# Optimization experiments

Measured on AMD Instinct MI355X. Metric: run time of the kernel, lower is better.

Reference implementation:

```python
import math
import jax, jax.numpy as jnp
import numpy as np

B, C, T, H, FC, L, K, S, O = 4, 512, 2048, 8, 2048, 6, 3, 256, 1
DK = C // H


def _conv1x1(x, w, b):
    # x: (B,Cin,T), w: (Cout,Cin)
    return jnp.einsum('oc,bct->bot', w, x) + b[None, :, None]


def _conv1d(x, w, b, pad):
    # x: (B,Cin,T), w: (Cout,Cin,K), pad: (left,right)
    y = jax.lax.conv_general_dilated(x, w, (1,), [pad],
                                     dimension_numbers=('NCH', 'OIH', 'NCH'))
    return y + b[None, :, None]


def _layernorm_c(x, g, b, eps=1e-5):
    # LayerNorm over channel dim (module transposes to put channels last)
    m = jnp.mean(x, axis=1, keepdims=True)
    v = jnp.mean((x - m) ** 2, axis=1, keepdims=True)
    return (x - m) * jax.lax.rsqrt(v + eps) * g[None, :, None] + b[None, :, None]


def _attention(x, qw, qb, kw, kb, vw, vb, ow, ob, tri):
    b_, c, t = x.shape
    # reshape(b, H, dk, t).transpose(2,3) -> (B,H,T,dk)
    q = _conv1x1(x, qw, qb).reshape(b_, H, DK, t).transpose(0, 1, 3, 2)
    k = _conv1x1(x, kw, kb).reshape(b_, H, DK, t).transpose(0, 1, 3, 2)
    v = _conv1x1(x, vw, vb).reshape(b_, H, DK, t).transpose(0, 1, 3, 2)
    scores = jnp.einsum('bhtd,bhsd->bhts', q, k) / math.sqrt(DK)
    scores = jnp.where(tri, scores, -1e4)  # causal mask, matches Tensor.where(mask, s, -10000)
    p = jax.nn.softmax(scores, axis=-1)
    o = jnp.einsum('bhts,bhsd->bhtd', p, v)
    o = o.transpose(0, 1, 3, 2).reshape(b_, c, t)
    return _conv1x1(o, ow, ob)


def _ffn(x, x_mask, w1, b1, w2, b2):
    # causal FFN: left pad K-1, activation=None -> relu, p_dropout=0
    y = _conv1d(x * x_mask, w1, b1, (K - 1, 0))
    y = jax.nn.relu(y)
    return _conv1d(y * x_mask, w2, b2, (K - 1, 0)) * x_mask


def _forward(x, norm_f0, x_mask, spk_emb,
             prenet_w, prenet_b, f0pre_w, f0pre_b, cond_w, cond_b, proj_w, proj_b,
             qw, qb, kw, kb, vw, vb, ow, ob,
             ln0_g, ln0_b, ln1_g, ln1_b,
             ffn1_w, ffn1_b, ffn2_w, ffn2_b):
    x = jax.lax.stop_gradient(x)  # torch.detach(x)
    x = x + _conv1x1(spk_emb, cond_w, cond_b)
    x = x + _conv1d(norm_f0, f0pre_w, f0pre_b, (1, 1))
    x = _conv1d(x, prenet_w, prenet_b, (1, 1)) * x_mask
    t = x.shape[2]
    tri = jnp.tril(jnp.ones((t, t), dtype=bool))[None, None]  # subsequent_mask
    x = x * x_mask
    for i in range(L):
        y = _attention(x, qw[i], qb[i], kw[i], kb[i], vw[i], vb[i], ow[i], ob[i], tri)
        x = _layernorm_c(x + y, ln0_g[i], ln0_b[i])
        y = _ffn(x, x_mask, ffn1_w[i], ffn1_b[i], ffn2_w[i], ffn2_b[i])
        x = _layernorm_c(x + y, ln1_g[i], ln1_b[i])
    x = x * x_mask
    return _conv1x1(x, proj_w, proj_b) * x_mask


def setup_inputs() -> dict:
    key = jax.random.key(0)
    ks = iter(jax.random.split(key, 40))
    rn = lambda shape, scale: jax.random.normal(next(ks), shape, jnp.float32) * scale
    inp = {
        'x': rn((B, C, T), 1.0),
        'norm_f0': rn((B, 1, T), 1.0),
        'x_mask': jnp.ones((B, 1, T), jnp.float32),
        'spk_emb': rn((B, S, T), 1.0),
        'prenet_w': rn((C, C, K), (C * K) ** -0.5), 'prenet_b': jnp.zeros((C,), jnp.float32),
        'f0pre_w': rn((C, 1, K), K ** -0.5), 'f0pre_b': jnp.zeros((C,), jnp.float32),
        'cond_w': rn((C, S), S ** -0.5), 'cond_b': jnp.zeros((C,), jnp.float32),
        'proj_w': rn((O, C), C ** -0.5), 'proj_b': jnp.zeros((O,), jnp.float32),
        'qw': rn((L, C, C), C ** -0.5), 'qb': jnp.zeros((L, C), jnp.float32),
        'kw': rn((L, C, C), C ** -0.5), 'kb': jnp.zeros((L, C), jnp.float32),
        'vw': rn((L, C, C), C ** -0.5), 'vb': jnp.zeros((L, C), jnp.float32),
        'ow': rn((L, C, C), C ** -0.5), 'ob': jnp.zeros((L, C), jnp.float32),
        'ln0_g': jnp.ones((L, C), jnp.float32), 'ln0_b': jnp.zeros((L, C), jnp.float32),
        'ln1_g': jnp.ones((L, C), jnp.float32), 'ln1_b': jnp.zeros((L, C), jnp.float32),
        'ffn1_w': rn((L, FC, C, K), (C * K) ** -0.5), 'ffn1_b': jnp.zeros((L, FC), jnp.float32),
        'ffn2_w': rn((L, C, FC, K), (FC * K) ** -0.5), 'ffn2_b': jnp.zeros((L, C), jnp.float32),
    }
    return inp


def reference(x, norm_f0, x_mask, spk_emb,
              prenet_w, prenet_b, f0pre_w, f0pre_b, cond_w, cond_b, proj_w, proj_b,
              qw, qb, kw, kb, vw, vb, ow, ob,
              ln0_g, ln0_b, ln1_g, ln1_b,
              ffn1_w, ffn1_b, ffn2_w, ffn2_b):
    return _forward(x, norm_f0, x_mask, spk_emb,
                    prenet_w, prenet_b, f0pre_w, f0pre_b, cond_w, cond_b, proj_w, proj_b,
                    qw, qb, kw, kb, vw, vb, ow, ob,
                    ln0_g, ln0_b, ln1_g, ln1_b,
                    ffn1_w, ffn1_b, ffn2_w, ffn2_b)
```

## Files before the change

kernel.cpp:

```cpp
#include <hip/hip_runtime.h>
#include <cstdint>
#include <cstddef>

#define T_LEN 2048
#define B_SZ 4
#define C_CH 512
#define H_N 8
#define DK_ 64
#define FC_CH 2048
#define L_N 6
#define KW 3
#define S_CH 256

typedef _Float16 h8 __attribute__((ext_vector_type(8)));
typedef _Float16 h4 __attribute__((ext_vector_type(4)));
typedef float floatx4 __attribute__((ext_vector_type(4)));

__global__ __launch_bounds__(256)
void cast_f16(const float* __restrict__ src, _Float16* __restrict__ dst, int n)
{
    int i = blockIdx.x * 256 + threadIdx.x;
    if (i < n) dst[i] = (_Float16)src[i];
}

__global__ __launch_bounds__(256)
void prepack_k3(const float* __restrict__ src, _Float16* __restrict__ dst,
                int Cin, int total)
{
    int i = blockIdx.x * 256 + threadIdx.x;
    if (i >= total) return;
    const int rk = Cin * 3;
    int row = i / rk, o = i - row * rk;
    int blk = o / 96, rr = o - blk * 96;
    int k = rr >> 5, cl = rr & 31;
    dst[i] = (_Float16)src[(size_t)row * rk + (size_t)(blk * 32 + cl) * 3 + k];
}

__global__ __launch_bounds__(256)
void prepack_qkv(const float* __restrict__ qw, const float* __restrict__ kw,
                 const float* __restrict__ vw, const float* __restrict__ qb,
                 const float* __restrict__ kb, const float* __restrict__ vb,
                 _Float16* __restrict__ dst, float* __restrict__ bdst)
{
    int i = blockIdx.x * 256 + threadIdx.x;
    const int total = L_N * 1536 * 512;
    if (i < total) {
        int l = i / (1536 * 512);
        int o = i - l * (1536 * 512);
        int m = o >> 9, c = o & 511;
        const float* s = (m < 512) ? qw : ((m < 1024) ? kw : vw);
        dst[i] = (_Float16)s[((size_t)l * 512 + (m & 511)) * 512 + c];
    }
    if (i < L_N * 1536) {
        int l = i / 1536, m = i - l * 1536;
        const float* s = (m < 512) ? qb : ((m < 1024) ? kb : vb);
        bdst[i] = s[l * 512 + (m & 511)];
    }
}

__global__ __launch_bounds__(256)
void transpose_f0(const float* __restrict__ src, _Float16* __restrict__ dst, int Cd,
                  const float* __restrict__ nf0, const float* __restrict__ f0w,
                  const float* __restrict__ f0b, int do_f0)
{
    __shared__ float tile[32][33];
    const int tl = threadIdx.x & 31;
    const int r  = threadIdx.x >> 5;
    const int t00 = blockIdx.x * 32;
    const int c00 = blockIdx.y * 32;
    const int b   = blockIdx.z;
    const float* s0 = src + (size_t)b * Cd * T_LEN;
#pragma unroll
    for (int rr = 0; rr < 4; ++rr) {
        int cl = r + rr * 8;
        tile[cl][tl] = s0[(size_t)(c00 + cl) * T_LEN + t00 + tl];
    }
    __syncthreads();
    _Float16* d0 = dst + (size_t)b * T_LEN * Cd;
    const int cg = c00 + tl;
#pragma unroll
    for (int rr = 0; rr < 4; ++rr) {
        int tlo = r + rr * 8;
        float v = tile[tl][tlo];
        if (do_f0) {
            int tg = t00 + tlo;
            float a = f0b[cg];
#pragma unroll
            for (int k = 0; k < 3; ++k) {
                int gt = tg + k - 1;
                if (gt >= 0 && gt < T_LEN) a += f0w[cg * 3 + k] * nf0[(size_t)b * T_LEN + gt];
            }
            v += a;
        }
        d0[(size_t)(t00 + tlo) * Cd + cg] = (_Float16)v;
    }
}

template<int KK, int OUTMODE>
__global__ __launch_bounds__(256)
void conv_gemm_mfma(const _Float16* __restrict__ in, const _Float16* __restrict__ Wpk,
                    const float* __restrict__ bias, const _Float16* __restrict__ res,
                    const float* __restrict__ mask, _Float16* __restrict__ out_v,
                    _Float16* __restrict__ out2,
                    int Cin, int out_stride, int pl, int do_relu,
                    int mask_in, int mask_out)
{
    constexpr int CS   = (KK == 3) ? 32 : 64;
    constexpr int NSEC = (KK == 3) ? 3 : 2;
    constexpr int AST  = NSEC * 32 + 8;
    constexpr int HALO = (KK == 3) ? 2 : 0;
    constexpr int RB   = 128 + 2 * HALO;
    constexpr int BST  = CS + 8;
    constexpr int NAH  = NSEC * 2;
    constexpr int NTASK = RB * (CS / 16);
    __shared__ _Float16 sA[128 * AST];
    __shared__ _Float16 sB[RB * BST];

    const int tid = threadIdx.x;
    const int lane = tid & 63;
    const int wid = tid >> 6;
    const int wm = wid >> 1, wt = wid & 1;
    const int r = lane & 15, q4 = lane >> 4;
    const int t0 = blockIdx.x * 128;
    const int m0 = blockIdx.y * 128;
    const int b  = blockIdx.z;
    const float* mk = mask + (size_t)b * T_LEN;

    floatx4 acc[4][4];
#pragma unroll
    for (int i = 0; i < 4; ++i)
#pragma unroll
        for (int j = 0; j < 4; ++j)
#pragma unroll
            for (int c = 0; c < 4; ++c) acc[i][j][c] = 0.f;

    const int arow = (KK == 3) ? (tid & 127) : (tid >> 1);
    const int ah0  = (KK == 3) ? ((tid >> 7) * (NSEC * 16)) : ((tid & 1) * (NSEC * 16));
    const _Float16* ap = Wpk + (size_t)(m0 + arow) * Cin * KK + ah0;

    int brw[2], bcc[2];
    bool bex[2], bval[2];
    _Float16 bm[2];
    const _Float16* bq[2];
    h8 areg[NAH], breg0[2][2], breg1[2][2];
#pragma unroll
    for (int t2 = 0; t2 < 2; ++t2) {
        const int id = tid + t2 * 256;
        bex[t2] = (id < NTASK);
        int row, c16;
        if (KK == 3) { row = id % RB; c16 = (id / RB) * 16; }
        else         { row = id >> 2; c16 = (id & 3) * 16; }
        const int gt = t0 + row - HALO;
        bval[t2] = bex[t2] && gt >= 0 && gt < T_LEN;
        brw[t2] = row; bcc[t2] = c16;
        bm[t2] = (_Float16)((bval[t2] && mask_in) ? mk[gt] : 1.f);
        bq[t2] = in + (size_t)b * T_LEN * Cin + (size_t)gt * Cin + c16;
#pragma unroll
        for (int hh = 0; hh < 2; ++hh)
#pragma unroll
            for (int j = 0; j < 8; ++j) {
                breg0[t2][hh][j] = (_Float16)0.f;
                breg1[t2][hh][j] = (_Float16)0.f;
            }
    }
    const int nch = Cin / CS;
#pragma unroll
    for (int j = 0; j < NAH; ++j) areg[j] = *reinterpret_cast<const h8*>(ap + j * 8);
#pragma unroll
    for (int t2 = 0; t2 < 2; ++t2)
        if (bval[t2]) {
            breg0[t2][0] = *reinterpret_cast<const h8*>(bq[t2]);
            breg0[t2][1] = *reinterpret_cast<const h8*>(bq[t2] + 8);
            breg1[t2][0] = *reinterpret_cast<const h8*>(bq[t2] + CS);
            breg1[t2][1] = *reinterpret_cast<const h8*>(bq[t2] + CS + 8);
            bq[t2] += 2 * CS;
        }

    auto run_chunk = [&](h8 (&br)[2][2], int ci) {
        __syncthreads();
#pragma unroll
        for (int j = 0; j < NAH; ++j)
            *reinterpret_cast<h8*>(&sA[arow * AST + ah0 + j * 8]) = areg[j];
#pragma unroll
        for (int t2 = 0; t2 < 2; ++t2)
            if (bex[t2]) {
                *reinterpret_cast<h8*>(&sB[brw[t2] * BST + bcc[t2]]) = br[t2][0] * bm[t2];
                *reinterpret_cast<h8*>(&sB[brw[t2] * BST + bcc[t2] + 8]) = br[t2][1] * bm[t2];
            }
        __syncthreads();
        if (ci + 1 < nch) {
            ap += CS * KK;
#pragma unroll
            for (int j = 0; j < NAH; ++j) areg[j] = *reinterpret_cast<const h8*>(ap + j * 8);
        }
        if (ci + 2 < nch) {
#pragma unroll
            for (int t2 = 0; t2 < 2; ++t2)
                if (bval[t2]) {
                    br[t2][0] = *reinterpret_cast<const h8*>(bq[t2]);
                    br[t2][1] = *reinterpret_cast<const h8*>(bq[t2] + 8);
                    bq[t2] += CS;
                }
        }
#pragma unroll
        for (int sec = 0; sec < NSEC; ++sec) {
            h8 af[4], bf[4];
#pragma unroll
            for (int im = 0; im < 4; ++im)
                af[im] = *reinterpret_cast<const h8*>(&sA[(wm * 64 + im * 16 + r) * AST + sec * 32 + q4 * 8]);
            const int rb0 = (KK == 3) ? (wt * 64 + r + sec - pl + HALO) : (wt * 64 + r);
            const int cb0 = (KK == 3) ? 0 : sec * 32;
#pragma unroll
            for (int jt = 0; jt < 4; ++jt)
                bf[jt] = *reinterpret_cast<const h8*>(&sB[(rb0 + jt * 16) * BST + cb0 + q4 * 8]);
#pragma unroll
            for (int im = 0; im < 4; ++im)
#pragma unroll
                for (int jt = 0; jt < 4; ++jt)
                    acc[im][jt] = __builtin_amdgcn_mfma_f32_16x16x32_f16(af[im], bf[jt], acc[im][jt], 0, 0, 0);
        }
    };

    for (int ci = 0; ci < nch; ci += 2) {
        run_chunk(breg0, ci);
        run_chunk(breg1, ci + 1);
    }

#pragma unroll
    for (int im = 0; im < 4; ++im) {
        const int mb = m0 + wm * 64 + im * 16 + q4 * 4;
        const float4 bv = *reinterpret_cast<const float4*>(&bias[mb]);
#pragma unroll
        for (int jt = 0; jt < 4; ++jt) {
            const int t = t0 + wt * 64 + jt * 16 + r;
            float vv[4];
            vv[0] = acc[im][jt][0] + bv.x;
            vv[1] = acc[im][jt][1] + bv.y;
            vv[2] = acc[im][jt][2] + bv.z;
            vv[3] = acc[im][jt][3] + bv.w;
            if (do_relu) {
#pragma unroll
                for (int c = 0; c < 4; ++c) vv[c] = fmaxf(vv[c], 0.f);
            }
            if (mask_out) {
                const float mv = mk[t];
#pragma unroll
                for (int c = 0; c < 4; ++c) vv[c] *= mv;
            }
            if (OUTMODE == 1) {
                const size_t ob = ((size_t)b * T_LEN + t) * out_stride + mb;
                if (res) {
                    const h4 rv = *reinterpret_cast<const h4*>(&res[ob]);
#pragma unroll
                    for (int c = 0; c < 4; ++c) vv[c] += (float)rv[c];
                }
                h4 hv;
#pragma unroll
                for (int c = 0; c < 4; ++c) hv[c] = (_Float16)vv[c];
                *reinterpret_cast<h4*>(&out_v[ob]) = hv;
            } else {
                if (m0 < 1024) {
                    const size_t ob = ((size_t)b * T_LEN + t) * 1024 + mb;
                    h4 hv;
#pragma unroll
                    for (int c = 0; c < 4; ++c) hv[c] = (_Float16)vv[c];
                    *reinterpret_cast<h4*>(&out_v[ob]) = hv;
                } else {
#pragma unroll
                    for (int reg = 0; reg < 4; ++reg)
                        out2[((size_t)b * C_CH + (mb - 1024) + reg) * T_LEN + t] = (_Float16)vv[reg];
                }
            }
        }
    }
}

__global__ __launch_bounds__(256)
void flash_attn_mfma(const _Float16* __restrict__ qk, const _Float16* __restrict__ vt,
                     _Float16* __restrict__ o)
{
    __shared__ _Float16 sK[64 * 72];
    __shared__ _Float16 sVt[64 * 72];
    __shared__ _Float16 sP[128 * 72];
    const int tid = threadIdx.x;
    const int lane = tid & 63;
    const int w = tid >> 6;
    const int r = lane & 15, q4 = lane >> 4;
    const int qt0 = (int)(15 - blockIdx.x) * 128;
    const int h = blockIdx.y, b = blockIdx.z;
    const size_t tb = (size_t)b * T_LEN;
    const int hq = h * 64, hk = 512 + h * 64;
    const _Float16* vbase = vt + ((size_t)b * C_CH + h * 64) * T_LEN;

    h8 qf[2][2];
#pragma unroll
    for (int im = 0; im < 2; ++im)
#pragma unroll
        for (int dc = 0; dc < 2; ++dc) {
            h8 t = *reinterpret_cast<const h8*>(
                &qk[(tb + qt0 + w * 32 + im * 16 + r) * 1024 + hq + dc * 32 + q4 * 8]);
            qf[im][dc] = t * (_Float16)0.125f;
        }

    floatx4 oacc[2][4];
    float mrow[2][4], lrow[2][4];
#pragma unroll
    for (int im = 0; im < 2; ++im)
#pragma unroll
        for (int reg = 0; reg < 4; ++reg) {
            mrow[im][reg] = -__builtin_inff();
            lrow[im][reg] = 0.f;
        }
#pragma unroll
    for (int im = 0; im < 2; ++im)
#pragma unroll
        for (int jd = 0; jd < 4; ++jd)
#pragma unroll
            for (int c = 0; c < 4; ++c) oacc[im][jd][c] = 0.f;

    const int qhi = qt0 + w * 32 + 31;
    const int nk = (qt0 >> 6) + 2;
    for (int kt = 0; kt < nk; ++kt) {
        const int kt0 = kt * 64;
        __syncthreads();
        {
            int row = tid >> 2, c16 = (tid & 3) * 16;
            const _Float16* src = &qk[(tb + kt0 + row) * 1024 + hk + c16];
            *reinterpret_cast<h8*>(&sK[row * 72 + c16]) = *reinterpret_cast<const h8*>(src);
            *reinterpret_cast<h8*>(&sK[row * 72 + c16 + 8]) = *reinterpret_cast<const h8*>(src + 8);
        }
#pragma unroll
        for (int p = 0; p < 2; ++p) {
            int id = p * 256 + tid;
            int d = id >> 3, s8 = (id & 7) * 8;
            *reinterpret_cast<h8*>(&sVt[d * 72 + s8]) =
                *reinterpret_cast<const h8*>(&vbase[(size_t)d * T_LEN + kt0 + s8]);
        }
        __syncthreads();
        if (kt0 <= qhi) {
            floatx4 sacc[2][4];
#pragma unroll
            for (int im = 0; im < 2; ++im)
#pragma unroll
                for (int js = 0; js < 4; ++js)
#pragma unroll
                    for (int c = 0; c < 4; ++c) sacc[im][js][c] = 0.f;
#pragma unroll
            for (int dc = 0; dc < 2; ++dc) {
                h8 kf[4];
#pragma unroll
                for (int js = 0; js < 4; ++js)
                    kf[js] = *reinterpret_cast<const h8*>(&sK[(js * 16 + r) * 72 + dc * 32 + q4 * 8]);
#pragma unroll
                for (int im = 0; im < 2; ++im)
#pragma unroll
                    for (int js = 0; js < 4; ++js)
                        sacc[im][js] = __builtin_amdgcn_mfma_f32_16x16x32_f16(qf[im][dc], kf[js], sacc[im][js], 0, 0, 0);
            }
#pragma unroll
            for (int im = 0; im < 2; ++im)
#pragma unroll
                for (int js = 0; js < 4; ++js) {
                    const int s_g = kt0 + js * 16 + r;
#pragma unroll
                    for (int reg = 0; reg < 4; ++reg) {
                        const int q_g = qt0 + w * 32 + im * 16 + q4 * 4 + reg;
                        if (s_g > q_g) sacc[im][js][reg] = -1e4f;
                    }
                }
            float mt[2][4];
#pragma unroll
            for (int im = 0; im < 2; ++im)
#pragma unroll
                for (int reg = 0; reg < 4; ++reg) {
                    float m0v = fmaxf(fmaxf(sacc[im][0][reg], sacc[im][1][reg]),
                                      fmaxf(sacc[im][2][reg], sacc[im][3][reg]));
#pragma unroll
                    for (int off = 1; off < 16; off <<= 1)
                        m0v = fmaxf(m0v, __shfl_xor(m0v, off));
                    mt[im][reg] = m0v;
                }
            float alpha[2][4];
#pragma unroll
            for (int im = 0; im < 2; ++im)
#pragma unroll
                for (int reg = 0; reg < 4; ++reg) {
                    float mn = fmaxf(mrow[im][reg], mt[im][reg]);
                    alpha[im][reg] = __expf(mrow[im][reg] - mn);
                    mrow[im][reg] = mn;
                    float rs = 0.f;
#pragma unroll
                    for (int js = 0; js < 4; ++js) {
                        float p = __expf(sacc[im][js][reg] - mn);
                        sacc[im][js][reg] = p;
                        rs += p;
                    }
#pragma unroll
                    for (int off = 1; off < 16; off <<= 1)
                        rs += __shfl_xor(rs, off);
                    lrow[im][reg] = lrow[im][reg] * alpha[im][reg] + rs;
                }
#pragma unroll
            for (int im = 0; im < 2; ++im)
#pragma unroll
                for (int jd = 0; jd < 4; ++jd)
#pragma unroll
                    for (int reg = 0; reg < 4; ++reg)
                        oacc[im][jd][reg] *= alpha[im][reg];
#pragma unroll
            for (int im = 0; im < 2; ++im)
#pragma unroll
                for (int js = 0; js < 4; ++js)
#pragma unroll
                    for (int reg = 0; reg < 4; ++reg)
                        sP[(w * 32 + im * 16 + q4 * 4 + reg) * 72 + js * 16 + r] =
                            (_Float16)sacc[im][js][reg];
#pragma unroll
            for (int sc = 0; sc < 2; ++sc) {
                h8 pf[2], vf[4];
#pragma unroll
                for (int im = 0; im < 2; ++im)
                    pf[im] = *reinterpret_cast<const h8*>(&sP[(w * 32 + im * 16 + r) * 72 + sc * 32 + q4 * 8]);
#pragma unroll
                for (int jd = 0; jd < 4; ++jd)
                    vf[jd] = *reinterpret_cast<const h8*>(&sVt[(jd * 16 + r) * 72 + sc * 32 + q4 * 8]);
#pragma unroll
                for (int im = 0; im < 2; ++im)
#pragma unroll
                    for (int jd = 0; jd < 4; ++jd)
                        oacc[im][jd] = __builtin_amdgcn_mfma_f32_16x16x32_f16(pf[im], vf[jd], oacc[im][jd], 0, 0, 0);
            }
        }
    }
#pragma unroll
    for (int im = 0; im < 2; ++im)
#pragma unroll
        for (int reg = 0; reg < 4; ++reg) {
            const float inv = 1.f / lrow[im][reg];
            const size_t rowb = (tb + qt0 + w * 32 + im * 16 + q4 * 4 + reg) * 512 + h * 64 + r;
#pragma unroll
            for (int jd = 0; jd < 4; ++jd)
                o[rowb + jd * 16] = (_Float16)(oacc[im][jd][reg] * inv);
        }
}

__global__ __launch_bounds__(256)
void ln_kernel(const _Float16* __restrict__ x, const _Float16* __restrict__ y,
               const float* __restrict__ g, const float* __restrict__ be,
               _Float16* __restrict__ outx)
{
    const int w = threadIdx.x >> 6, lane = threadIdx.x & 63;
    const int t = blockIdx.x * 4 + w, b = blockIdx.y;
    const size_t base = ((size_t)b * T_LEN + t) * C_CH + lane * 8;
    h8 xv = *reinterpret_cast<const h8*>(&x[base]);
    h8 yv = *reinterpret_cast<const h8*>(&y[base]);
    float v[8];
#pragma unroll
    for (int i = 0; i < 8; ++i) v[i] = (float)xv[i] + (float)yv[i];
    float s = 0.f, s2 = 0.f;
#pragma unroll
    for (int i = 0; i < 8; ++i) { s += v[i]; s2 += v[i] * v[i]; }
#pragma unroll
    for (int off = 1; off < 64; off <<= 1) {
        s  += __shfl_xor(s, off);
        s2 += __shfl_xor(s2, off);
    }
    const float mean = s * (1.f / C_CH);
    const float var  = s2 * (1.f / C_CH) - mean * mean;
    const float rstd = rsqrtf(var + 1e-5f);
    float4 g0 = *reinterpret_cast<const float4*>(&g[lane * 8]);
    float4 g1 = *reinterpret_cast<const float4*>(&g[lane * 8 + 4]);
    float4 b0 = *reinterpret_cast<const float4*>(&be[lane * 8]);
    float4 b1 = *reinterpret_cast<const float4*>(&be[lane * 8 + 4]);
    const float gg[8] = {g0.x, g0.y, g0.z, g0.w, g1.x, g1.y, g1.z, g1.w};
    const float bb[8] = {b0.x, b0.y, b0.z, b0.w, b1.x, b1.y, b1.z, b1.w};
    h8 ov;
#pragma unroll
    for (int i = 0; i < 8; ++i)
        ov[i] = (_Float16)((v[i] - mean) * rstd * gg[i] + bb[i]);
    *reinterpret_cast<h8*>(&outx[base]) = ov;
}

__global__ __launch_bounds__(256)
void proj_kernel(const _Float16* __restrict__ x, const float* __restrict__ pw,
                 const float* __restrict__ pb, const float* __restrict__ mask,
                 float* __restrict__ out)
{
    const int w = threadIdx.x >> 6, lane = threadIdx.x & 63;
    const int t = blockIdx.x * 4 + w, b = blockIdx.y;
    const size_t base = ((size_t)b * T_LEN + t) * C_CH + lane * 8;
    h8 xv = *reinterpret_cast<const h8*>(&x[base]);
    float4 p0 = *reinterpret_cast<const float4*>(&pw[lane * 8]);
    float4 p1 = *reinterpret_cast<const float4*>(&pw[lane * 8 + 4]);
    const float pp[8] = {p0.x, p0.y, p0.z, p0.w, p1.x, p1.y, p1.z, p1.w};
    float s = 0.f;
#pragma unroll
    for (int i = 0; i < 8; ++i) s += (float)xv[i] * pp[i];
#pragma unroll
    for (int off = 1; off < 64; off <<= 1) s += __shfl_xor(s, off);
    if (lane == 0) {
        const float mv = mask[(size_t)b * T_LEN + t];
        out[(size_t)b * T_LEN + t] = (s * mv + pb[0]) * mv;
    }
}

extern "C" void kernel_launch(void* const* d_in, const int* in_sizes, int n_in,
                              void* d_out, int out_size, void* d_ws, size_t ws_size,
                              hipStream_t stream)
{
    const float* x    = (const float*)d_in[0];
    const float* nf0  = (const float*)d_in[1];
    const float* xm   = (const float*)d_in[2];
    const float* spk  = (const float*)d_in[3];
    const float* prw  = (const float*)d_in[4];
    const float* prb  = (const float*)d_in[5];
    const float* f0w  = (const float*)d_in[6];
    const float* f0b  = (const float*)d_in[7];
    const float* cw   = (const float*)d_in[8];
    const float* cb   = (const float*)d_in[9];
    const float* pjw  = (const float*)d_in[10];
    const float* pjb  = (const float*)d_in[11];
    const float* qw   = (const float*)d_in[12];
    const float* qb   = (const float*)d_in[13];
    const float* kw   = (const float*)d_in[14];
    const float* kb   = (const float*)d_in[15];
    const float* vw   = (const float*)d_in[16];
    const float* vb   = (const float*)d_in[17];
    const float* ow   = (const float*)d_in[18];
    const float* ob   = (const float*)d_in[19];
    const float* ln0g = (const float*)d_in[20];
    const float* ln0b = (const float*)d_in[21];
    const float* ln1g = (const float*)d_in[22];
    const float* ln1b = (const float*)d_in[23];
    const float* f1w  = (const float*)d_in[24];
    const float* f1b  = (const float*)d_in[25];
    const float* f2w  = (const float*)d_in[26];
    const float* f2b  = (const float*)d_in[27];
    float* out = (float*)d_out;

    const size_t NCT = (size_t)B_SZ * C_CH * T_LEN;
    char* wp = (char*)d_ws;
    _Float16* xbuf = (_Float16*)wp; wp += NCT * 2;
    _Float16* t0h  = (_Float16*)wp; wp += NCT * 2;
    _Float16* qk   = (_Float16*)wp; wp += NCT * 4;
    _Float16* vt   = (_Float16*)wp; wp += NCT * 2;
    _Float16* obf  = (_Float16*)wp; wp += NCT * 2;
    _Float16* h1   = (_Float16*)wp; wp += NCT * 8;
    _Float16* xT   = h1;
    _Float16* spkT = obf;
    _Float16* Wqkv = (_Float16*)wp; wp += (size_t)L_N * 1536 * 512 * 2;
    _Float16* Wo   = (_Float16*)wp; wp += (size_t)L_N * 512 * 512 * 2;
    _Float16* Wcnd = (_Float16*)wp; wp += (size_t)512 * 256 * 2;
    _Float16* Wpre = (_Float16*)wp; wp += (size_t)512 * 512 * 3 * 2;
    _Float16* Wf1  = (_Float16*)wp; wp += (size_t)L_N * 2048 * 512 * 3 * 2;
    _Float16* Wf2  = (_Float16*)wp; wp += (size_t)L_N * 512 * 2048 * 3 * 2;
    float*    Bqkv = (float*)wp;    wp += (size_t)L_N * 1536 * 4;

    dim3 blk(256);
    dim3 gC(16, 4, B_SZ);
    dim3 gQKV(16, 12, B_SZ);
    dim3 gF(16, 16, B_SZ);
    dim3 gAT(16, H_N, B_SZ);
    dim3 gLN(T_LEN / 4, B_SZ);

    {
        int n;
        n = C_CH * S_CH;            cast_f16<<<(n + 255) / 256, blk, 0, stream>>>(cw, Wcnd, n);
        n = L_N * C_CH * C_CH;      cast_f16<<<(n + 255) / 256, blk, 0, stream>>>(ow, Wo, n);
        n = C_CH * C_CH * 3;        prepack_k3<<<(n + 255) / 256, blk, 0, stream>>>(prw, Wpre, C_CH, n);
        n = L_N * FC_CH * C_CH * 3; prepack_k3<<<(n + 255) / 256, blk, 0, stream>>>(f1w, Wf1, C_CH, n);
        n = L_N * C_CH * FC_CH * 3; prepack_k3<<<(n + 255) / 256, blk, 0, stream>>>(f2w, Wf2, FC_CH, n);
        n = L_N * 1536 * 512;       prepack_qkv<<<(n + 255) / 256, blk, 0, stream>>>(qw, kw, vw, qb, kb, vb, Wqkv, Bqkv);
    }

    transpose_f0<<<dim3(64, 16, B_SZ), blk, 0, stream>>>(x, xT, C_CH, nf0, f0w, f0b, 1);
    transpose_f0<<<dim3(64, 8, B_SZ), blk, 0, stream>>>(spk, spkT, S_CH, nullptr, nullptr, nullptr, 0);
    conv_gemm_mfma<1, 1><<<gC, blk, 0, stream>>>(spkT, Wcnd, cb, xT, xm, t0h, nullptr, S_CH, C_CH, 0, 0, 0, 0);
    conv_gemm_mfma<3, 1><<<gC, blk, 0, stream>>>(t0h, Wpre, prb, nullptr, xm, xbuf, nullptr, C_CH, C_CH, 1, 0, 0, 1);

    for (int l = 0; l < L_N; ++l) {
        const size_t bo = (size_t)l * C_CH;
        conv_gemm_mfma<1, 3><<<gQKV, blk, 0, stream>>>(xbuf, Wqkv + (size_t)l * 1536 * 512, Bqkv + l * 1536,
                                                       nullptr, xm, qk, vt, C_CH, 1024, 0, 0, 0, 0);
        flash_attn_mfma<<<gAT, blk, 0, stream>>>(qk, vt, obf);
        conv_gemm_mfma<1, 1><<<gC, blk, 0, stream>>>(obf, Wo + (size_t)l * 512 * 512, ob + bo,
                                                     nullptr, xm, t0h, nullptr, C_CH, C_CH, 0, 0, 0, 0);
        ln_kernel<<<gLN, blk, 0, stream>>>(xbuf, t0h, ln0g + bo, ln0b + bo, xbuf);
        conv_gemm_mfma<3, 1><<<gF, blk, 0, stream>>>(xbuf, Wf1 + (size_t)l * FC_CH * C_CH * 3, f1b + (size_t)l * FC_CH,
                                                     nullptr, xm, h1, nullptr, C_CH, FC_CH, 2, 1, 1, 0);
        conv_gemm_mfma<3, 1><<<gC, blk, 0, stream>>>(h1, Wf2 + (size_t)l * C_CH * FC_CH * 3, f2b + bo,
                                                     nullptr, xm, t0h, nullptr, FC_CH, C_CH, 2, 0, 1, 1);
        ln_kernel<<<gLN, blk, 0, stream>>>(xbuf, t0h, ln1g + bo, ln1b + bo, xbuf);
    }
    proj_kernel<<<gLN, blk, 0, stream>>>(xbuf, pjw, pjb, xm, out);
}
```

Before: 2.476 ms.

## Shrink flash-attention query tile to 64 and compute transposed scores

The flash attention kernel now handles 64 query rows per block instead of 128, giving twice as many blocks and one 16-row MFMA tile per wave. Scores are computed as K·Q^T, so each lane owns one query column and row max and sum need only two cross-lane shuffles instead of four-step reductions per row. The P tile is written to shared memory as packed 4-element vectors, and the causal skip check is dropped because the loop bound now stops exactly at the diagonal tile. In exchange, each K/V tile loaded into shared memory is reused by half as many query rows, which doubles K/V traffic, and extra shuffles are needed to broadcast the rescale factors.

```diff
diff --git a/kernel.cpp b/kernel.cpp
--- a/kernel.cpp
+++ b/kernel.cpp
@@ -281,45 +281,35 @@
 {
     __shared__ _Float16 sK[64 * 72];
     __shared__ _Float16 sVt[64 * 72];
-    __shared__ _Float16 sP[128 * 72];
+    __shared__ _Float16 sP[64 * 72];
     const int tid = threadIdx.x;
     const int lane = tid & 63;
     const int w = tid >> 6;
     const int r = lane & 15, q4 = lane >> 4;
-    const int qt0 = (int)(15 - blockIdx.x) * 128;
+    const int qt0 = (int)(31 - blockIdx.x) * 64;
     const int h = blockIdx.y, b = blockIdx.z;
     const size_t tb = (size_t)b * T_LEN;
     const int hq = h * 64, hk = 512 + h * 64;
     const _Float16* vbase = vt + ((size_t)b * C_CH + h * 64) * T_LEN;
 
-    h8 qf[2][2];
-#pragma unroll
-    for (int im = 0; im < 2; ++im)
-#pragma unroll
-        for (int dc = 0; dc < 2; ++dc) {
-            h8 t = *reinterpret_cast<const h8*>(
-                &qk[(tb + qt0 + w * 32 + im * 16 + r) * 1024 + hq + dc * 32 + q4 * 8]);
-            qf[im][dc] = t * (_Float16)0.125f;
-        }
-
-    floatx4 oacc[2][4];
-    float mrow[2][4], lrow[2][4];
-#pragma unroll
-    for (int im = 0; im < 2; ++im)
-#pragma unroll
-        for (int reg = 0; reg < 4; ++reg) {
-            mrow[im][reg] = -__builtin_inff();
-            lrow[im][reg] = 0.f;
-        }
-#pragma unroll
-    for (int im = 0; im < 2; ++im)
-#pragma unroll
-        for (int jd = 0; jd < 4; ++jd)
-#pragma unroll
-            for (int c = 0; c < 4; ++c) oacc[im][jd][c] = 0.f;
-
-    const int qhi = qt0 + w * 32 + 31;
-    const int nk = (qt0 >> 6) + 2;
+    h8 qf[2];
+#pragma unroll
+    for (int dc = 0; dc < 2; ++dc) {
+        h8 t = *reinterpret_cast<const h8*>(
+            &qk[(tb + qt0 + w * 16 + r) * 1024 + hq + dc * 32 + q4 * 8]);
+        qf[dc] = t * (_Float16)0.125f;
+    }
+
+    floatx4 oacc[4];
+    float mrow = -__builtin_inff();
+    float lrow = 0.f;
+#pragma unroll
+    for (int jd = 0; jd < 4; ++jd)
+#pragma unroll
+        for (int c = 0; c < 4; ++c) oacc[jd][c] = 0.f;
+
+    const int qg = qt0 + w * 16 + r;
+    const int nk = (qt0 >> 6) + 1;
     for (int kt = 0; kt < nk; ++kt) {
         const int kt0 = kt * 64;
         __syncthreads();
@@ -337,111 +327,91 @@
                 *reinterpret_cast<const h8*>(&vbase[(size_t)d * T_LEN + kt0 + s8]);
         }
         __syncthreads();
-        if (kt0 <= qhi) {
-            floatx4 sacc[2][4];
-#pragma unroll
-            for (int im = 0; im < 2; ++im)
-#pragma unroll
-                for (int js = 0; js < 4; ++js)
-#pragma unroll
-                    for (int c = 0; c < 4; ++c) sacc[im][js][c] = 0.f;
-#pragma unroll
-            for (int dc = 0; dc < 2; ++dc) {
-                h8 kf[4];
-#pragma unroll
-                for (int js = 0; js < 4; ++js)
-                    kf[js] = *reinterpret_cast<const h8*>(&sK[(js * 16 + r) * 72 + dc * 32 + q4 * 8]);
-#pragma unroll
-                for (int im = 0; im < 2; ++im)
-#pragma unroll
-                    for (int js = 0; js < 4; ++js)
-                        sacc[im][js] = __builtin_amdgcn_mfma_f32_16x16x32_f16(qf[im][dc], kf[js], sacc[im][js], 0, 0, 0);
-            }
-#pragma unroll
-            for (int im = 0; im < 2; ++im)
-#pragma unroll
-                for (int js = 0; js < 4; ++js) {
-                    const int s_g = kt0 + js * 16 + r;
-#pragma unroll
-                    for (int reg = 0; reg < 4; ++reg) {
-                        const int q_g = qt0 + w * 32 + im * 16 + q4 * 4 + reg;
-                        if (s_g > q_g) sacc[im][js][reg] = -1e4f;
-                    }
-                }
-            float mt[2][4];
-#pragma unroll
-            for (int im = 0; im < 2; ++im)
-#pragma unroll
-                for (int reg = 0; reg < 4; ++reg) {
-                    float m0v = fmaxf(fmaxf(sacc[im][0][reg], sacc[im][1][reg]),
-                                      fmaxf(sacc[im][2][reg], sacc[im][3][reg]));
-#pragma unroll
-                    for (int off = 1; off < 16; off <<= 1)
-                        m0v = fmaxf(m0v, __shfl_xor(m0v, off));
-                    mt[im][reg] = m0v;
-                }
-            float alpha[2][4];
-#pragma unroll
-            for (int im = 0; im < 2; ++im)
-#pragma unroll
-                for (int reg = 0; reg < 4; ++reg) {
-                    float mn = fmaxf(mrow[im][reg], mt[im][reg]);
-                    alpha[im][reg] = __expf(mrow[im][reg] - mn);
-                    mrow[im][reg] = mn;
-                    float rs = 0.f;
-#pragma unroll
-                    for (int js = 0; js < 4; ++js) {
-                        float p = __expf(sacc[im][js][reg] - mn);
-                        sacc[im][js][reg] = p;
-                        rs += p;
-                    }
-#pragma unroll
-                    for (int off = 1; off < 16; off <<= 1)
-                        rs += __shfl_xor(rs, off);
-                    lrow[im][reg] = lrow[im][reg] * alpha[im][reg] + rs;
-                }
-#pragma unroll
-            for (int im = 0; im < 2; ++im)
-#pragma unroll
-                for (int jd = 0; jd < 4; ++jd)
-#pragma unroll
-                    for (int reg = 0; reg < 4; ++reg)
-                        oacc[im][jd][reg] *= alpha[im][reg];
-#pragma unroll
-            for (int im = 0; im < 2; ++im)
-#pragma unroll
-                for (int js = 0; js < 4; ++js)
-#pragma unroll
-                    for (int reg = 0; reg < 4; ++reg)
-                        sP[(w * 32 + im * 16 + q4 * 4 + reg) * 72 + js * 16 + r] =
-                            (_Float16)sacc[im][js][reg];
-#pragma unroll
-            for (int sc = 0; sc < 2; ++sc) {
-                h8 pf[2], vf[4];
-#pragma unroll
-                for (int im = 0; im < 2; ++im)
-                    pf[im] = *reinterpret_cast<const h8*>(&sP[(w * 32 + im * 16 + r) * 72 + sc * 32 + q4 * 8]);
-#pragma unroll
-                for (int jd = 0; jd < 4; ++jd)
-                    vf[jd] = *reinterpret_cast<const h8*>(&sVt[(jd * 16 + r) * 72 + sc * 32 + q4 * 8]);
-#pragma unroll
-                for (int im = 0; im < 2; ++im)
-#pragma unroll
-                    for (int jd = 0; jd < 4; ++jd)
-                        oacc[im][jd] = __builtin_amdgcn_mfma_f32_16x16x32_f16(pf[im], vf[jd], oacc[im][jd], 0, 0, 0);
-            }
-        }
-    }
-#pragma unroll
-    for (int im = 0; im < 2; ++im)
-#pragma unroll
-        for (int reg = 0; reg < 4; ++reg) {
-            const float inv = 1.f / lrow[im][reg];
-            const size_t rowb = (tb + qt0 + w * 32 + im * 16 + q4 * 4 + reg) * 512 + h * 64 + r;
+
+        floatx4 sacc[4];
+#pragma unroll
+        for (int js = 0; js < 4; ++js)
+#pragma unroll
+            for (int c = 0; c < 4; ++c) sacc[js][c] = 0.f;
+#pragma unroll
+        for (int dc = 0; dc < 2; ++dc) {
+            h8 kf[4];
+#pragma unroll
+            for (int js = 0; js < 4; ++js)
+                kf[js] = *reinterpret_cast<const h8*>(&sK[(js * 16 + r) * 72 + dc * 32 + q4 * 8]);
+#pragma unroll
+            for (int js = 0; js < 4; ++js)
+                sacc[js] = __builtin_amdgcn_mfma_f32_16x16x32_f16(kf[js], qf[dc], sacc[js], 0, 0, 0);
+        }
+#pragma unroll
+        for (int js = 0; js < 4; ++js) {
+            const int sb = kt0 + js * 16 + q4 * 4;
+#pragma unroll
+            for (int reg = 0; reg < 4; ++reg)
+                if (sb + reg > qg) sacc[js][reg] = -1e4f;
+        }
+        float mt;
+        {
+            float a = fmaxf(fmaxf(sacc[0][0], sacc[0][1]), fmaxf(sacc[0][2], sacc[0][3]));
+            float bm = fmaxf(fmaxf(sacc[1][0], sacc[1][1]), fmaxf(sacc[1][2], sacc[1][3]));
+            float c = fmaxf(fmaxf(sacc[2][0], sacc[2][1]), fmaxf(sacc[2][2], sacc[2][3]));
+            float d = fmaxf(fmaxf(sacc[3][0], sacc[3][1]), fmaxf(sacc[3][2], sacc[3][3]));
+            mt = fmaxf(fmaxf(a, bm), fmaxf(c, d));
+        }
+        mt = fmaxf(mt, __shfl_xor(mt, 16));
+        mt = fmaxf(mt, __shfl_xor(mt, 32));
+        const float mn = fmaxf(mrow, mt);
+        const float alpha = __expf(mrow - mn);
+        mrow = mn;
+        float rs = 0.f;
+#pragma unroll
+        for (int js = 0; js < 4; ++js)
+#pragma unroll
+            for (int reg = 0; reg < 4; ++reg) {
+                float p = __expf(sacc[js][reg] - mn);
+                sacc[js][reg] = p;
+                rs += p;
+            }
+        rs += __shfl_xor(rs, 16);
+        rs += __shfl_xor(rs, 32);
+        lrow = lrow * alpha + rs;
+        float ao[4];
+#pragma unroll
+        for (int reg = 0; reg < 4; ++reg) ao[reg] = __shfl(alpha, (q4 << 2) + reg, 16);
+#pragma unroll
+        for (int jd = 0; jd < 4; ++jd)
+#pragma unroll
+            for (int reg = 0; reg < 4; ++reg) oacc[jd][reg] *= ao[reg];
+#pragma unroll
+        for (int js = 0; js < 4; ++js) {
+            h4 hv;
+#pragma unroll
+            for (int reg = 0; reg < 4; ++reg) hv[reg] = (_Float16)sacc[js][reg];
+            *reinterpret_cast<h4*>(&sP[(w * 16 + r) * 72 + js * 16 + q4 * 4]) = hv;
+        }
+#pragma unroll
+        for (int sc = 0; sc < 2; ++sc) {
+            h8 pf = *reinterpret_cast<const h8*>(&sP[(w * 16 + r) * 72 + sc * 32 + q4 * 8]);
+            h8 vf[4];
 #pragma unroll
             for (int jd = 0; jd < 4; ++jd)
-                o[rowb + jd * 16] = (_Float16)(oacc[im][jd][reg] * inv);
-        }
+                vf[jd] = *reinterpret_cast<const h8*>(&sVt[(jd * 16 + r) * 72 + sc * 32 + q4 * 8]);
+#pragma unroll
+            for (int jd = 0; jd < 4; ++jd)
+                oacc[jd] = __builtin_amdgcn_mfma_f32_16x16x32_f16(pf, vf[jd], oacc[jd], 0, 0, 0);
+        }
+    }
+    const float linv = 1.f / lrow;
+    float li[4];
+#pragma unroll
+    for (int reg = 0; reg < 4; ++reg) li[reg] = __shfl(linv, (q4 << 2) + reg, 16);
+#pragma unroll
+    for (int reg = 0; reg < 4; ++reg) {
+        const size_t rowb = (tb + qt0 + w * 16 + (q4 << 2) + reg) * 512 + h * 64 + r;
+#pragma unroll
+        for (int jd = 0; jd < 4; ++jd)
+            o[rowb + jd * 16] = (_Float16)(oacc[jd][reg] * li[reg]);
+    }
 }
 
 __global__ __launch_bounds__(256)
@@ -560,7 +530,7 @@
     dim3 gC(16, 4, B_SZ);
     dim3 gQKV(16, 12, B_SZ);
     dim3 gF(16, 16, B_SZ);
-    dim3 gAT(16, H_N, B_SZ);
+    dim3 gAT(32, H_N, B_SZ);
     dim3 gLN(T_LEN / 4, B_SZ);
 
     {
```

After: 2.243 ms. -9.4%, faster.
